# Performance work log

Measured on AMD Instinct MI355X. Metric: run time of the kernel, lower is better.

The kernel has to match this reference:

```python
import jax, jax.numpy as jnp
import numpy as np

EMB = 256
HID = 1024
N_TRACKS = 4096
SEQ = 9
SCALE = 4.0


def setup_inputs() -> dict:
    key = jax.random.key(0)
    ks = jax.random.split(key, 12)

    def init(k, shape, fan_in):
        b = 1.0 / np.sqrt(fan_in)
        return jax.random.uniform(k, shape, jnp.float32, -b, b)

    return {
        "observed": jax.random.normal(ks[0], (SEQ, N_TRACKS, 2), jnp.float32),
        "emb_w": init(ks[1], (EMB - 2, 2), 2),
        "emb_b": init(ks[2], (EMB - 2,), 2),
        "enc_wih": init(ks[3], (4 * HID, EMB), HID),
        "enc_whh": init(ks[4], (4 * HID, HID), HID),
        "enc_b": init(ks[5], (4 * HID,), HID),
        "dec_wih": init(ks[6], (4 * HID, EMB), HID),
        "dec_whh": init(ks[7], (4 * HID, HID), HID),
        "dec_b": init(ks[8], (4 * HID,), HID),
        "h2n_w": init(ks[9], (5, HID), HID),
        "h2n_b": init(ks[10], (5,), HID),
        "n_predict": 12,
    }


def _forward(observed, emb_w, emb_b, enc_wih, enc_whh, enc_b,
             dec_wih, dec_whh, dec_b, h2n_w, h2n_b, n_predict):
    n = observed.shape[1]
    H = enc_whh.shape[1]
    E = enc_wih.shape[1]

    def cell(x, h, c, wih, whh, b):
        # PyTorch LSTMCell gate order: i, f, g, o
        g = x @ wih.T + h @ whh.T + b
        i, f, gg, o = jnp.split(g, 4, axis=-1)
        c = jax.nn.sigmoid(f) * c + jax.nn.sigmoid(i) * jnp.tanh(gg)
        h = jax.nn.sigmoid(o) * jnp.tanh(c)
        return h, c

    def embed(v):
        # Linear(2, E-2) -> ReLU, then 2 zero tag channels
        e = jax.nn.relu((v * SCALE) @ emb_w.T + emb_b)
        return jnp.concatenate([e, jnp.zeros((v.shape[0], 2), e.dtype)], axis=1)

    def h2n(h):
        raw = h @ h2n_w.T + h2n_b
        sig = 0.01 + 0.2 * jax.nn.sigmoid(raw[:, 2:4])  # sigma1, sigma2
        rho = 0.7 * jax.nn.sigmoid(raw[:, 4:5])          # rho
        return jnp.concatenate([raw[:, :2], sig, rho], axis=1)

    def step(params, h, c, obs1, obs2):
        wih, whh, b = params
        mask = ~(jnp.isnan(obs1[:, 0]) | jnp.isnan(obs2[:, 0]))  # [N]
        x = embed(obs2 - obs1)
        h2, c2 = cell(x, h, c, wih, whh, b)
        nrm = h2n(h2)
        m = mask[:, None]
        h = jnp.where(m, h2, h)
        c = jnp.where(m, c2, c)
        normal = jnp.where(m, nrm, jnp.nan)
        pos = obs2 + normal[:, :2]
        return h, c, normal, pos

    h = jnp.zeros((n, H), observed.dtype)
    c = jnp.zeros((n, H), observed.dtype)

    # encoder start tag
    tag_enc = jnp.zeros((n, E), observed.dtype).at[:, -2].set(1.0)
    h, c = cell(tag_enc, h, c, enc_wih, enc_whh, enc_b)

    enc_p = (enc_wih, enc_whh, enc_b)

    def enc_scan(carry, obs_pair):
        h, c = carry
        o1, o2 = obs_pair
        h, c, normal, pos = step(enc_p, h, c, o1, o2)
        return (h, c), (normal, pos)

    (h, c), (enc_normals, enc_positions) = jax.lax.scan(
        enc_scan, (h, c), (observed[:-1], observed[1:]))

    # decoder start tag
    tag_dec = jnp.zeros((n, E), observed.dtype).at[:, -1].set(1.0)
    h, c = cell(tag_dec, h, c, dec_wih, dec_whh, dec_b)

    dec_p = (dec_wih, dec_whh, dec_b)
    p1, p2 = enc_positions[-2], enc_positions[-1]

    def dec_scan(carry, _):
        h, c, p1, p2 = carry
        o1 = jax.lax.stop_gradient(p1)  # .detach() in torch
        o2 = jax.lax.stop_gradient(p2)
        h, c, normal, pos = step(dec_p, h, c, o1, o2)
        return (h, c, p2, pos), (normal, pos)

    _, (dec_normals, dec_positions) = jax.lax.scan(
        dec_scan, (h, c, p1, p2), None, length=n_predict - 1)

    rel_pred_scene = jnp.concatenate([enc_normals, dec_normals], axis=0)
    pred_scene = jnp.concatenate([enc_positions, dec_positions], axis=0)
    return rel_pred_scene, pred_scene


def reference(observed, emb_w, emb_b, enc_wih, enc_whh, enc_b,
              dec_wih, dec_whh, dec_b, h2n_w, h2n_b, n_predict):
    return _forward(observed, emb_w, emb_b, enc_wih, enc_whh, enc_b,
                    dec_wih, dec_whh, dec_b, h2n_w, h2n_b, n_predict)
```

## Files before the change

### kernel.cpp

```cpp
#include <hip/hip_runtime.h>
#include <stdint.h>

#define NTRK 4096
#define HIDN 1024
#define EMBN 256
#define KTOT 1280
#define NOUT 19

typedef __attribute__((ext_vector_type(8))) short short8;
typedef __attribute__((ext_vector_type(4))) float f32x4;

typedef __attribute__((address_space(1))) const void GV;
typedef __attribute__((address_space(3))) void LV;

__device__ __forceinline__ uint16_t f2bf(float f) {
  uint32_t u = __float_as_uint(f);
  u += 0x7fffu + ((u >> 16) & 1u);
  return (uint16_t)(u >> 16);
}
__device__ __forceinline__ float bf2f(uint16_t v) {
  return __uint_as_float(((uint32_t)v) << 16);
}
__device__ __forceinline__ float sigm(float x) { return 1.0f / (1.0f + expf(-x)); }
__device__ __forceinline__ float sigmf_(float x) {
  return __builtin_amdgcn_rcpf(1.0f + __expf(-x));
}
__device__ __forceinline__ float tanhf_(float x) {
  return 2.0f * __builtin_amdgcn_rcpf(1.0f + __expf(-2.0f * x)) - 1.0f;
}

__global__ __launch_bounds__(256) void prep_weights(
    const float* __restrict__ encWih, const float* __restrict__ encWhh,
    const float* __restrict__ encB,
    const float* __restrict__ decWih, const float* __restrict__ decWhh,
    const float* __restrict__ decB,
    uint16_t* __restrict__ WcatE, uint16_t* __restrict__ WcatD,
    float* __restrict__ biasE, float* __restrict__ biasD, float* __restrict__ biasDT)
{
  const int jp = blockIdx.x;
  const int q = jp >> 6, r = jp & 63;
  const int gate = r >> 4, l16 = r & 15;
  const int u = q * 16 + l16;
  const int orig = gate * 1024 + u;
  const int t = threadIdx.x;

  WcatE[(size_t)jp * KTOT + t] = f2bf(encWih[(size_t)orig * 256 + t]);
  WcatD[(size_t)jp * KTOT + t] = f2bf(decWih[(size_t)orig * 256 + t]);
#pragma unroll
  for (int c = 0; c < 4; c++) {
    WcatE[(size_t)jp * KTOT + 256 + c * 256 + t] = f2bf(encWhh[(size_t)orig * 1024 + c * 256 + t]);
    WcatD[(size_t)jp * KTOT + 256 + c * 256 + t] = f2bf(decWhh[(size_t)orig * 1024 + c * 256 + t]);
  }
  if (t == 0) {
    biasE[jp]  = encB[orig];
    biasD[jp]  = decB[orig];
    biasDT[jp] = decB[orig] + decWih[(size_t)orig * 256 + 255];
  }
}

__global__ void init_h0(const float* __restrict__ encWih, const float* __restrict__ encB,
                        float* __restrict__ h0, float* __restrict__ c0)
{
  const int u = blockIdx.x * 256 + threadIdx.x;
  if (u >= 1024) return;
  const float gi = encWih[(size_t)(u) * 256 + 254]        + encB[u];
  const float gg = encWih[(size_t)(2048 + u) * 256 + 254] + encB[2048 + u];
  const float go = encWih[(size_t)(3072 + u) * 256 + 254] + encB[3072 + u];
  const float c = sigm(gi) * tanhf(gg);
  c0[u] = c;
  h0[u] = sigm(go) * tanhf(c);
}

__global__ void fill_state(const float* __restrict__ h0, const float* __restrict__ c0,
                           uint16_t* __restrict__ H, float* __restrict__ Cst)
{
  const size_t i = (size_t)blockIdx.x * 256 + threadIdx.x;
  const int u = (int)(i & 1023);
  H[i] = f2bf(h0[u]);
  Cst[i] = c0[u];
}

__global__ __launch_bounds__(256) void embed_k(
    const float* __restrict__ o1, const float* __restrict__ o2,
    const float* __restrict__ ew, const float* __restrict__ eb,
    uint16_t* __restrict__ X)
{
  const int trk = blockIdx.x;
  const int j = threadIdx.x;
  const float vx = (o2[trk * 2]     - o1[trk * 2])     * 4.0f;
  const float vy = (o2[trk * 2 + 1] - o1[trk * 2 + 1]) * 4.0f;
  float e = 0.f;
  if (j < 254) e = fmaxf(vx * ew[j * 2] + vy * ew[j * 2 + 1] + eb[j], 0.f);
  X[(size_t)trk * 256 + j] = f2bf(e);
}

__global__ __launch_bounds__(256) void embed8(
    const float* __restrict__ observed, const float* __restrict__ ew,
    const float* __restrict__ eb, uint16_t* __restrict__ Xall)
{
  const int t = blockIdx.y;
  const int trk = blockIdx.x;
  const int j = threadIdx.x;
  const float* o1 = observed + ((size_t)t * 4096 + trk) * 2;
  const float* o2 = o1 + 4096 * 2;
  const float vx = (o2[0] - o1[0]) * 4.0f;
  const float vy = (o2[1] - o1[1]) * 4.0f;
  float e = 0.f;
  if (j < 254) e = fmaxf(vx * ew[j * 2] + vy * ew[j * 2 + 1] + eb[j], 0.f);
  Xall[((size_t)t * 4096 + trk) * 256 + j] = f2bf(e);
}

__global__ __launch_bounds__(512, 4) void gemm_lstm(
    const uint16_t* __restrict__ X,    const uint16_t* __restrict__ Hin,
    const uint16_t* __restrict__ Wcat, const float* __restrict__ bias,
    float* __restrict__ Cst,           uint16_t* __restrict__ Hout,
    const float* __restrict__ obs1,    const float* __restrict__ obs2,
    int k0, int maskmode)
{
  __shared__ uint16_t As[3 * 4096];
  __shared__ uint16_t Bs[3 * 8192];
  __shared__ uint8_t  smask[128];

  const int tid  = threadIdx.x;
  const int w    = tid >> 6;
  const int lane = tid & 63;
  const int wr   = w >> 2;
  const int wc   = w & 3;
  const int quad = lane >> 4;
  const int l15  = lane & 15;

  const int bid = blockIdx.y * 16 + blockIdx.x;
  const int xcd = bid & 7;
  const int j   = bid >> 3;
  const int bmS = (xcd >> 2) * 16 + (j >> 2);
  const int bnS = (xcd & 3) * 4 + (j & 3);
  const int bm  = bmS * 128;
  const int bn  = bnS * 256;

  const int NT = (KTOT - k0) >> 5;

  if (tid < 128) {
    bool m = true;
    if (maskmode) {
      const float a = obs1[(bm + tid) * 2];
      const float b = obs2[(bm + tid) * 2];
      m = !((a != a) || (b != b));
    }
    smask[tid] = m ? 1 : 0;
  }

  const int srow = w * 16 + (lane >> 2);
  const int sch  = ((lane & 3) ^ ((lane >> 3) & 3)) * 8;
  const uint16_t* pXr = X ? X + (size_t)(bm + srow) * 256 + sch : (const uint16_t*)0;
  const uint16_t* pHr = Hin  + (size_t)(bm + srow) * 1024 + sch;
  const uint16_t* pWr = Wcat + (size_t)(bn + srow) * (size_t)KTOT + sch;

  auto stage = [&](int V, int slot) {
    if (V >= NT) return;
    const int kg = k0 + V * 32;
    uint16_t* ad = As + slot * 4096 + w * 16 * 32;
    if (kg < 256) {
      __builtin_amdgcn_global_load_lds((GV*)(pXr + kg),         (LV*)ad, 16, 0, 0);
    } else {
      __builtin_amdgcn_global_load_lds((GV*)(pHr + (kg - 256)), (LV*)ad, 16, 0, 0);
    }
    uint16_t* bd = Bs + slot * 8192 + w * 16 * 32;
    __builtin_amdgcn_global_load_lds((GV*)(pWr + kg),                        (LV*)bd,          16, 0, 0);
    __builtin_amdgcn_global_load_lds((GV*)(pWr + (size_t)128 * KTOT + kg),   (LV*)(bd + 4096), 16, 0, 0);
  };

  f32x4 acc[4][4];
#pragma unroll
  for (int i = 0; i < 4; i++)
#pragma unroll
    for (int n = 0; n < 4; n++) acc[i][n] = (f32x4){0.f, 0.f, 0.f, 0.f};

  stage(0, 0); stage(1, 1);
  asm volatile("s_waitcnt vmcnt(3)" ::: "memory");
  __builtin_amdgcn_s_barrier();

  const int cc = (quad ^ ((l15 >> 1) & 3)) * 8;

  int sT = 0;
  for (int T = 0; T < NT; T++) {
    const int sS = (sT == 0) ? 2 : sT - 1;
    const uint16_t* Ab = As + sT * 4096;
    const uint16_t* Bb = Bs + sT * 8192;
    short8 a[4], b[4];
#pragma unroll
    for (int i = 0; i < 4; i++)
      a[i] = *(const short8*)(Ab + (wr * 64 + i * 16 + l15) * 32 + cc);
#pragma unroll
    for (int n = 0; n < 4; n++)
      b[n] = *(const short8*)(Bb + (wc * 64 + n * 16 + l15) * 32 + cc);
    stage(T + 2, sS);
    __builtin_amdgcn_s_setprio(1);
#pragma unroll
    for (int i = 0; i < 4; i++)
#pragma unroll
      for (int n = 0; n < 4; n++)
        acc[i][n] = __builtin_amdgcn_mfma_f32_16x16x32_bf16(a[i], b[n], acc[i][n], 0, 0, 0);
    __builtin_amdgcn_s_setprio(0);
    if (T < NT - 2) {
      asm volatile("s_waitcnt vmcnt(3)" ::: "memory");
    } else {
      asm volatile("s_waitcnt vmcnt(0)" ::: "memory");
    }
    __builtin_amdgcn_s_barrier();
    sT = (sT == 2) ? 0 : sT + 1;
  }

  const int u  = ((bn >> 6) + wc) * 16 + l15;
  const int jb = bn + wc * 64 + l15;
  const float b_i = bias[jb];
  const float b_f = bias[jb + 16];
  const float b_g = bias[jb + 32];
  const float b_o = bias[jb + 48];

#pragma unroll
  for (int i = 0; i < 4; i++) {
#pragma unroll
    for (int r = 0; r < 4; r++) {
      const int row = bm + wr * 64 + i * 16 + quad * 4 + r;
      const size_t idx = (size_t)row * 1024 + u;
      uint16_t hv;
      if (smask[row - bm]) {
        const float gi = acc[i][0][r] + b_i;
        const float gf = acc[i][1][r] + b_f;
        const float gg = acc[i][2][r] + b_g;
        const float go = acc[i][3][r] + b_o;
        const float cn = sigmf_(gf) * Cst[idx] + sigmf_(gi) * tanhf_(gg);
        Cst[idx] = cn;
        hv = f2bf(sigmf_(go) * tanhf_(cn));
      } else {
        hv = Hin[idx];
      }
      Hout[idx] = hv;
    }
  }
}

__global__ __launch_bounds__(256) void h2n_pos(
    const uint16_t* __restrict__ H, const float* __restrict__ w5, const float* __restrict__ b5,
    const float* __restrict__ obs1, const float* __restrict__ obs2,
    float* __restrict__ outrel, float* __restrict__ outpos,
    const float* __restrict__ pprev, const float* __restrict__ ew,
    const float* __restrict__ eb, uint16_t* __restrict__ Xnext, int do_embed)
{
  const int lane  = threadIdx.x & 63;
  const int track = blockIdx.x * 4 + (threadIdx.x >> 6);

  const uint16_t* hrow = H + (size_t)track * 1024 + lane * 16;
  const short8 v0 = *(const short8*)(hrow);
  const short8 v1 = *(const short8*)(hrow + 8);
  float hv[16];
#pragma unroll
  for (int j = 0; j < 8; j++) {
    hv[j]     = bf2f((uint16_t)v0[j]);
    hv[8 + j] = bf2f((uint16_t)v1[j]);
  }
  const int kb = lane * 16;
  float p[5];
#pragma unroll
  for (int o = 0; o < 5; o++) {
    const float* wr = w5 + (size_t)o * 1024 + kb;
    float s = 0.f;
#pragma unroll
    for (int j = 0; j < 16; j++) s += hv[j] * wr[j];
    p[o] = s;
  }
#pragma unroll
  for (int o = 0; o < 5; o++) {
    float v = p[o];
    v += __shfl_xor(v, 32); v += __shfl_xor(v, 16); v += __shfl_xor(v, 8);
    v += __shfl_xor(v, 4);  v += __shfl_xor(v, 2);  v += __shfl_xor(v, 1);
    p[o] = v;
  }
  const float o1x = obs1[track * 2];
  const float o2x = obs2[track * 2];
  const float o2y = obs2[track * 2 + 1];
  const bool msk = !((o1x != o1x) || (o2x != o2x));
  float n0 = p[0] + b5[0];
  float n1 = p[1] + b5[1];
  float n2 = 0.01f + 0.2f * sigmf_(p[2] + b5[2]);
  float n3 = 0.01f + 0.2f * sigmf_(p[3] + b5[3]);
  float n4 = 0.7f  * sigmf_(p[4] + b5[4]);
  if (!msk) {
    const float qn = __uint_as_float(0x7fc00000u);
    n0 = n1 = n2 = n3 = n4 = qn;
  }
  const float posx = o2x + n0;
  const float posy = o2y + n1;
  if (lane == 0) {
    float* rr = outrel + (size_t)track * 5;
    rr[0] = n0; rr[1] = n1; rr[2] = n2; rr[3] = n3; rr[4] = n4;
    outpos[track * 2]     = posx;
    outpos[track * 2 + 1] = posy;
  }
  if (do_embed) {
    const float vx = (posx - pprev[track * 2])     * 4.0f;
    const float vy = (posy - pprev[track * 2 + 1]) * 4.0f;
    uint16_t* xr = Xnext + (size_t)track * 256;
#pragma unroll
    for (int ii = 0; ii < 4; ii++) {
      const int j = ii * 64 + lane;
      float e = 0.f;
      if (j < 254) e = fmaxf(vx * ew[j * 2] + vy * ew[j * 2 + 1] + eb[j], 0.f);
      xr[j] = f2bf(e);
    }
  }
}

extern "C" void kernel_launch(void* const* d_in, const int* in_sizes, int n_in,
                              void* d_out, int out_size, void* d_ws, size_t ws_size,
                              hipStream_t stream)
{
  const float* observed = (const float*)d_in[0];
  const float* emb_w    = (const float*)d_in[1];
  const float* emb_b    = (const float*)d_in[2];
  const float* enc_wih  = (const float*)d_in[3];
  const float* enc_whh  = (const float*)d_in[4];
  const float* enc_b    = (const float*)d_in[5];
  const float* dec_wih  = (const float*)d_in[6];
  const float* dec_whh  = (const float*)d_in[7];
  const float* dec_b    = (const float*)d_in[8];
  const float* h2n_w    = (const float*)d_in[9];
  const float* h2n_b    = (const float*)d_in[10];

  char* ws = (char*)d_ws;
  size_t off = 0;
  auto alloc = [&](size_t bytes) -> void* {
    size_t cur = (off + 255) & ~(size_t)255;
    off = cur + bytes;
    return (void*)(ws + cur);
  };
  uint16_t* WcatE = (uint16_t*)alloc((size_t)4096 * KTOT * 2);
  uint16_t* WcatD = (uint16_t*)alloc((size_t)4096 * KTOT * 2);
  float*    biasE = (float*)alloc(4096 * 4);
  float*    biasD = (float*)alloc(4096 * 4);
  float*    biasDT= (float*)alloc(4096 * 4);
  float*    h0    = (float*)alloc(1024 * 4);
  float*    c0    = (float*)alloc(1024 * 4);
  uint16_t* HA    = (uint16_t*)alloc((size_t)4096 * 1024 * 2);
  uint16_t* HB    = (uint16_t*)alloc((size_t)4096 * 1024 * 2);
  float*    Cst   = (float*)alloc((size_t)4096 * 1024 * 4);
  uint16_t* Xb    = (uint16_t*)alloc((size_t)4096 * 256 * 2);
  const size_t xall_bytes = (size_t)8 * 4096 * 256 * 2;
  const bool use_xall = (off + 256 + xall_bytes) <= ws_size;
  uint16_t* Xall = use_xall ? (uint16_t*)alloc(xall_bytes) : nullptr;

  float* outrel = (float*)d_out;
  float* outpos = outrel + (size_t)NOUT * 4096 * 5;

  prep_weights<<<4096, 256, 0, stream>>>(enc_wih, enc_whh, enc_b, dec_wih, dec_whh, dec_b,
                                         WcatE, WcatD, biasE, biasD, biasDT);
  init_h0<<<4, 256, 0, stream>>>(enc_wih, enc_b, h0, c0);
  fill_state<<<16384, 256, 0, stream>>>(h0, c0, HA, Cst);
  if (use_xall) {
    embed8<<<dim3(4096, 8), 256, 0, stream>>>(observed, emb_w, emb_b, Xall);
  }

  uint16_t* Hin = HA;
  uint16_t* Hout = HB;
  const dim3 ggrid(16, 32);

  for (int t = 0; t < 8; t++) {
    const float* o1 = observed + (size_t)t * 4096 * 2;
    const float* o2 = observed + (size_t)(t + 1) * 4096 * 2;
    uint16_t* Xt = Xb;
    if (use_xall) {
      Xt = Xall + (size_t)t * 4096 * 256;
    } else {
      embed_k<<<4096, 256, 0, stream>>>(o1, o2, emb_w, emb_b, Xb);
    }
    gemm_lstm<<<ggrid, 512, 0, stream>>>(Xt, Hin, WcatE, biasE, Cst, Hout, o1, o2, 0, 1);
    const int de = (t == 7) ? 1 : 0;
    h2n_pos<<<1024, 256, 0, stream>>>(Hout, h2n_w, h2n_b, o1, o2,
                                      outrel + (size_t)t * 4096 * 5,
                                      outpos + (size_t)t * 4096 * 2,
                                      outpos + (size_t)6 * 4096 * 2, emb_w, emb_b, Xb, de);
    uint16_t* tmp = Hin; Hin = Hout; Hout = tmp;
  }

  gemm_lstm<<<ggrid, 512, 0, stream>>>(nullptr, Hin, WcatD, biasDT, Cst, Hout,
                                       nullptr, nullptr, 256, 0);
  { uint16_t* tmp = Hin; Hin = Hout; Hout = tmp; }

  for (int s = 0; s < 11; s++) {
    const float* p1 = outpos + (size_t)(6 + s) * 4096 * 2;
    const float* p2 = outpos + (size_t)(7 + s) * 4096 * 2;
    gemm_lstm<<<ggrid, 512, 0, stream>>>(Xb, Hin, WcatD, biasD, Cst, Hout, p1, p2, 0, 1);
    const int de = (s < 10) ? 1 : 0;
    h2n_pos<<<1024, 256, 0, stream>>>(Hout, h2n_w, h2n_b, p1, p2,
                                      outrel + (size_t)(8 + s) * 4096 * 5,
                                      outpos + (size_t)(8 + s) * 4096 * 2,
                                      p2, emb_w, emb_b, Xb, de);
    uint16_t* tmp = Hin; Hin = Hout; Hout = tmp;
  }
}
```

Measured before the change: 1.257 ms.

## Load the A operand straight into registers with double buffering, bypassing LDS

The activation (A) tile is no longer staged through shared memory. Each wave now loads its MFMA A fragments from global memory into registers, one k-step ahead, alternating between two register buffers. The weight (B) tile keeps its three-slot LDS pipeline, with the vmcnt waits renumbered for the new load counts. This removes the A-side LDS writes and reads and frees LDS, at the cost of the four column-waves loading the same A rows separately. It also adds more register pressure and depends on the compiler's waitcnt placement for the register loads.

```diff
diff --git a/kernel.cpp b/kernel.cpp
--- a/kernel.cpp
+++ b/kernel.cpp
@@ -117,7 +117,6 @@
     const float* __restrict__ obs1,    const float* __restrict__ obs2,
     int k0, int maskmode)
 {
-  __shared__ uint16_t As[3 * 4096];
   __shared__ uint16_t Bs[3 * 8192];
   __shared__ uint8_t  smask[128];
 
@@ -151,22 +150,32 @@
 
   const int srow = w * 16 + (lane >> 2);
   const int sch  = ((lane & 3) ^ ((lane >> 3) & 3)) * 8;
-  const uint16_t* pXr = X ? X + (size_t)(bm + srow) * 256 + sch : (const uint16_t*)0;
-  const uint16_t* pHr = Hin  + (size_t)(bm + srow) * 1024 + sch;
   const uint16_t* pWr = Wcat + (size_t)(bn + srow) * (size_t)KTOT + sch;
 
-  auto stage = [&](int V, int slot) {
+  auto stageB = [&](int V, int slot) {
     if (V >= NT) return;
     const int kg = k0 + V * 32;
-    uint16_t* ad = As + slot * 4096 + w * 16 * 32;
+    uint16_t* bd = Bs + slot * 8192 + w * 16 * 32;
+    __builtin_amdgcn_global_load_lds((GV*)(pWr + kg),                      (LV*)bd,          16, 0, 0);
+    __builtin_amdgcn_global_load_lds((GV*)(pWr + (size_t)128 * KTOT + kg), (LV*)(bd + 4096), 16, 0, 0);
+  };
+
+  const int arow = bm + wr * 64 + l15;
+  const uint16_t* aX = X ? (X + (size_t)arow * 256 + quad * 8) : (const uint16_t*)0;
+  const uint16_t* aH = Hin + (size_t)arow * 1024 + quad * 8;
+
+  auto loadA = [&](int V, short8 (&A)[4]) {
+    if (V >= NT) return;
+    const int kg = k0 + V * 32;
     if (kg < 256) {
-      __builtin_amdgcn_global_load_lds((GV*)(pXr + kg),         (LV*)ad, 16, 0, 0);
+#pragma unroll
+      for (int i = 0; i < 4; i++)
+        A[i] = *(const short8*)(aX + kg + i * 16 * 256);
     } else {
-      __builtin_amdgcn_global_load_lds((GV*)(pHr + (kg - 256)), (LV*)ad, 16, 0, 0);
-    }
-    uint16_t* bd = Bs + slot * 8192 + w * 16 * 32;
-    __builtin_amdgcn_global_load_lds((GV*)(pWr + kg),                        (LV*)bd,          16, 0, 0);
-    __builtin_amdgcn_global_load_lds((GV*)(pWr + (size_t)128 * KTOT + kg),   (LV*)(bd + 4096), 16, 0, 0);
+#pragma unroll
+      for (int i = 0; i < 4; i++)
+        A[i] = *(const short8*)(aH + (kg - 256) + i * 16 * 1024);
+    }
   };
 
   f32x4 acc[4][4];
@@ -175,39 +184,45 @@
 #pragma unroll
     for (int n = 0; n < 4; n++) acc[i][n] = (f32x4){0.f, 0.f, 0.f, 0.f};
 
-  stage(0, 0); stage(1, 1);
-  asm volatile("s_waitcnt vmcnt(3)" ::: "memory");
+  short8 A0[4], A1[4];
+
+  stageB(0, 0); stageB(1, 1);
+  loadA(0, A0);
+  asm volatile("s_waitcnt vmcnt(4)" ::: "memory");
   __builtin_amdgcn_s_barrier();
 
   const int cc = (quad ^ ((l15 >> 1) & 3)) * 8;
 
-  int sT = 0;
-  for (int T = 0; T < NT; T++) {
-    const int sS = (sT == 0) ? 2 : sT - 1;
-    const uint16_t* Ab = As + sT * 4096;
-    const uint16_t* Bb = Bs + sT * 8192;
-    short8 a[4], b[4];
-#pragma unroll
-    for (int i = 0; i < 4; i++)
-      a[i] = *(const short8*)(Ab + (wr * 64 + i * 16 + l15) * 32 + cc);
+  int sc = 0;
+  auto body = [&](int T, short8 (&Ac)[4], short8 (&An)[4]) {
+    loadA(T + 1, An);
+    int s2 = sc + 2; if (s2 >= 3) s2 -= 3;
+    stageB(T + 2, s2);
+    const uint16_t* Bb = Bs + sc * 8192;
+    short8 b[4];
 #pragma unroll
     for (int n = 0; n < 4; n++)
       b[n] = *(const short8*)(Bb + (wc * 64 + n * 16 + l15) * 32 + cc);
-    stage(T + 2, sS);
     __builtin_amdgcn_s_setprio(1);
 #pragma unroll
     for (int i = 0; i < 4; i++)
 #pragma unroll
       for (int n = 0; n < 4; n++)
-        acc[i][n] = __builtin_amdgcn_mfma_f32_16x16x32_bf16(a[i], b[n], acc[i][n], 0, 0, 0);
+        acc[i][n] = __builtin_amdgcn_mfma_f32_16x16x32_bf16(Ac[i], b[n], acc[i][n], 0, 0, 0);
     __builtin_amdgcn_s_setprio(0);
     if (T < NT - 2) {
-      asm volatile("s_waitcnt vmcnt(3)" ::: "memory");
-    } else {
-      asm volatile("s_waitcnt vmcnt(0)" ::: "memory");
-    }
-    __builtin_amdgcn_s_barrier();
-    sT = (sT == 2) ? 0 : sT + 1;
+      asm volatile("s_waitcnt vmcnt(6)" ::: "memory");
+      __builtin_amdgcn_s_barrier();
+    } else if (T == NT - 2) {
+      asm volatile("s_waitcnt vmcnt(4)" ::: "memory");
+      __builtin_amdgcn_s_barrier();
+    }
+    sc = sc + 1; if (sc >= 3) sc -= 3;
+  };
+
+  for (int T = 0; T < NT; T += 2) {
+    body(T, A0, A1);
+    body(T + 1, A1, A0);
   }
 
   const int u  = ((bn >> 6) + wc) * 16 + l15;
```

New measurement: 2.329 ms. 1.85x slower.
